# Kernel optimization log

Hardware: AMD Instinct MI355X
Metric: run time of the kernel (lower is better)

## Reference

```python
import jax, jax.numpy as jnp
import numpy as np
import math

B, S, H, NH, NKV, D, I, LCK = 2, 1024, 2048, 32, 8, 64, 8192, 3
EPS = 1e-6
THETA = 10000.0


def rms_norm(x, w, eps=EPS):
    xf = x.astype(jnp.float32)
    var = jnp.mean(xf * xf, axis=-1, keepdims=True)
    return (w * (xf * jax.lax.rsqrt(var + eps))).astype(x.dtype)


def rotate_half(x):
    d = x.shape[-1] // 2
    return jnp.concatenate([-x[..., d:], x[..., :d]], axis=-1)


def setup_inputs() -> dict:
    key = jax.random.key(0)
    ks = jax.random.split(key, 16)
    sc = 0.02
    inp = {
        'input_emb': jax.random.normal(ks[0], (B, S, H), jnp.float32),
        'hidden_states': jax.random.normal(ks[1], (B, S, H), jnp.float32),
        'cache_k': jax.random.normal(ks[2], (LCK, B, NH, S, D), jnp.float32),
        'cache_v': jax.random.normal(ks[3], (LCK, B, NH, S, D), jnp.float32),
    }
    neg = jnp.finfo(jnp.float32).min
    causal = jnp.where(jnp.tril(jnp.ones((S, S), bool)), 0.0, neg).astype(jnp.float32)
    inp['attention_mask'] = jnp.broadcast_to(causal[None, None], (B, 1, S, S))
    inp['position_ids'] = jnp.broadcast_to(jnp.arange(S, dtype=jnp.int32)[None], (B, S))
    inp['wq'] = jax.random.normal(ks[4], (NH * D, 2 * H), jnp.float32) * sc
    inp['wk'] = jax.random.normal(ks[5], (NKV * D, 2 * H), jnp.float32) * sc
    inp['wv'] = jax.random.normal(ks[6], (NKV * D, 2 * H), jnp.float32) * sc
    inp['wo'] = jax.random.normal(ks[7], (H, NH * D), jnp.float32) * sc
    inp['w_gate'] = jax.random.normal(ks[8], (I, H), jnp.float32) * sc
    inp['w_up'] = jax.random.normal(ks[9], (I, H), jnp.float32) * sc
    inp['w_down'] = jax.random.normal(ks[10], (H, I), jnp.float32) * sc
    inp['hidden_norm_w'] = jnp.ones((H,), jnp.float32)
    inp['input_ln_w'] = jnp.ones((H,), jnp.float32)
    inp['post_ln_w'] = jnp.ones((H,), jnp.float32)
    return inp


def _forward(input_emb, hidden_states, cache_k, cache_v, attention_mask, position_ids,
             wq, wk, wv, wo, w_gate, w_up, w_down, hidden_norm_w, input_ln_w, post_ln_w):
    residual = hidden_states
    h = rms_norm(hidden_states, hidden_norm_w)
    e = rms_norm(input_emb, input_ln_w)
    x = jnp.concatenate([e, h], axis=-1)  # [B,S,2H]

    q = jnp.einsum('bsi,oi->bso', x, wq).reshape(B, S, NH, D).transpose(0, 2, 1, 3)
    k = jnp.einsum('bsi,oi->bso', x, wk).reshape(B, S, NKV, D).transpose(0, 2, 1, 3)
    v = jnp.einsum('bsi,oi->bso', x, wv).reshape(B, S, NKV, D).transpose(0, 2, 1, 3)

    # RoPE table up to seq_len = S + LCK, indexed at position_ids + LCK
    inv_freq = 1.0 / (THETA ** (jnp.arange(0, D, 2, dtype=jnp.float32) / D))
    t = jnp.arange(S + LCK, dtype=jnp.float32)
    freqs = t[:, None] * inv_freq[None, :]
    emb = jnp.concatenate([freqs, freqs], axis=-1)  # [S+LCK, D]
    pos = position_ids + LCK
    cos = jnp.cos(emb)[pos][:, None]  # [B,1,S,D]
    sin = jnp.sin(emb)[pos][:, None]
    q = q * cos + rotate_half(q) * sin
    k = k * cos + rotate_half(k) * sin

    n_rep = NH // NKV
    k = jnp.repeat(k, n_rep, axis=1)  # [B,NH,S,D]
    v = jnp.repeat(v, n_rep, axis=1)

    scale = 1.0 / math.sqrt(D)
    # full causal attention against the oldest cache entry
    s0 = jnp.einsum('bhqd,bhkd->bhqk', q, cache_k[0]) * scale + attention_mask
    # diagonal (same-position) attention against remaining cache entries + current keys
    extra_k = jnp.concatenate([cache_k[1:], k[None]], axis=0)  # [LCK,B,NH,S,D]
    extra_v = jnp.concatenate([cache_v[1:], v[None]], axis=0)
    sd = jnp.einsum('bhqd,nbhqd->bhqn', q, extra_k) * scale  # [B,NH,S,LCK]

    attn = jax.nn.softmax(jnp.concatenate([s0, sd], axis=-1).astype(jnp.float32), axis=-1).astype(q.dtype)
    out = jnp.einsum('bhqk,bhkd->bhqd', attn[..., :S], cache_v[0])
    out = out + jnp.einsum('bhqn,nbhqd->bhqd', attn[..., S:], extra_v)
    out = out.transpose(0, 2, 1, 3).reshape(B, S, NH * D)
    attn_out = jnp.einsum('bsi,oi->bso', out, wo)

    h2 = residual + attn_out
    hn = rms_norm(h2, post_ln_w)
    mlp = jnp.einsum('bsi,oi->bso', jax.nn.silu(jnp.einsum('bsi,oi->bso', hn, w_gate)) * jnp.einsum('bsi,oi->bso', hn, w_up), w_down)
    return h2 + mlp


def reference(input_emb, hidden_states, cache_k, cache_v, attention_mask, position_ids,
              wq, wk, wv, wo, w_gate, w_up, w_down, hidden_norm_w, input_ln_w, post_ln_w):
    return _forward(input_emb, hidden_states, cache_k, cache_v, attention_mask, position_ids,
                    wq, wk, wv, wo, w_gate, w_up, w_down, hidden_norm_w, input_ln_w, post_ln_w)
```

## Files before the change

kernel.cpp:

```cpp
#include <hip/hip_runtime.h>
#include <math.h>

#define B_   2
#define S_   1024
#define H_   2048
#define NH_  32
#define NKV_ 8
#define D_   64
#define I_   8192
#define LCK_ 3
#define M_   (B_ * S_)

typedef unsigned short u16;
typedef unsigned int   u32;
typedef __attribute__((ext_vector_type(8))) short bf16x8;
typedef __attribute__((ext_vector_type(4))) float f32x4;
typedef __attribute__((ext_vector_type(2))) unsigned int u32x2;

__device__ __forceinline__ u16 f2b(float f) {
  u32 u = __float_as_uint(f);
  u += 0x7fffu + ((u >> 16) & 1u);
  return (u16)(u >> 16);
}
__device__ __forceinline__ float b2f(u16 h) { return __uint_as_float(((u32)h) << 16); }

__device__ __forceinline__ void st_bf4(u16* p, float a, float b, float c, float d) {
  u32x2 v;
  v.x = (u32)f2b(a) | ((u32)f2b(b) << 16);
  v.y = (u32)f2b(c) | ((u32)f2b(d) << 16);
  *(u32x2*)p = v;
}

__device__ __forceinline__ void cvt16(const float4& a, const float4& b,
                                      const float4& c, const float4& d,
                                      bf16x8& lo, bf16x8& hi) {
  lo[0] = (short)f2b(a.x); lo[1] = (short)f2b(a.y); lo[2] = (short)f2b(a.z); lo[3] = (short)f2b(a.w);
  lo[4] = (short)f2b(b.x); lo[5] = (short)f2b(b.y); lo[6] = (short)f2b(b.z); lo[7] = (short)f2b(b.w);
  hi[0] = (short)f2b(c.x); hi[1] = (short)f2b(c.y); hi[2] = (short)f2b(c.z); hi[3] = (short)f2b(c.w);
  hi[4] = (short)f2b(d.x); hi[5] = (short)f2b(d.y); hi[6] = (short)f2b(d.z); hi[7] = (short)f2b(d.w);
}

__device__ __forceinline__ void async16(const void* g, void* l) {
  __builtin_amdgcn_global_load_lds(
      (const __attribute__((address_space(1))) unsigned int*)(uintptr_t)g,
      (__attribute__((address_space(3))) unsigned int*)(unsigned int)(uintptr_t)l,
      16, 0, 0);
}

__global__ __launch_bounds__(256) void norm_concat_kernel(
    const float* __restrict__ emb, const float* __restrict__ hid,
    const float* __restrict__ w_e, const float* __restrict__ w_h,
    u16* __restrict__ x)
{
  const int row = blockIdx.x;
  const int t = threadIdx.x;
  const float* e = emb + (size_t)row * H_;
  const float* h = hid + (size_t)row * H_;

  const float4 ev0 = *(const float4*)&e[t * 4];
  const float4 ev1 = *(const float4*)&e[t * 4 + 1024];
  const float4 hv0 = *(const float4*)&h[t * 4];
  const float4 hv1 = *(const float4*)&h[t * 4 + 1024];

  float se = ev0.x*ev0.x + ev0.y*ev0.y + ev0.z*ev0.z + ev0.w*ev0.w
           + ev1.x*ev1.x + ev1.y*ev1.y + ev1.z*ev1.z + ev1.w*ev1.w;
  float sh = hv0.x*hv0.x + hv0.y*hv0.y + hv0.z*hv0.z + hv0.w*hv0.w
           + hv1.x*hv1.x + hv1.y*hv1.y + hv1.z*hv1.z + hv1.w*hv1.w;

  #pragma unroll
  for (int m = 1; m < 64; m <<= 1) {
    se += __shfl_xor(se, m);
    sh += __shfl_xor(sh, m);
  }
  __shared__ float red[8];
  const int wv = t >> 6;
  if ((t & 63) == 0) { red[wv] = se; red[4 + wv] = sh; }
  __syncthreads();
  se = red[0] + red[1] + red[2] + red[3];
  sh = red[4] + red[5] + red[6] + red[7];

  const float re = 1.0f / sqrtf(se * (1.0f / H_) + 1e-6f);
  const float rh = 1.0f / sqrtf(sh * (1.0f / H_) + 1e-6f);

  const float4 we0 = *(const float4*)&w_e[t * 4];
  const float4 we1 = *(const float4*)&w_e[t * 4 + 1024];
  const float4 wh0 = *(const float4*)&w_h[t * 4];
  const float4 wh1 = *(const float4*)&w_h[t * 4 + 1024];

  u16* xr = x + (size_t)row * (2 * H_);
  st_bf4(&xr[t * 4],        ev0.x*re*we0.x, ev0.y*re*we0.y, ev0.z*re*we0.z, ev0.w*re*we0.w);
  st_bf4(&xr[t * 4 + 1024], ev1.x*re*we1.x, ev1.y*re*we1.y, ev1.z*re*we1.z, ev1.w*re*we1.w);
  st_bf4(&xr[2048 + t * 4],        hv0.x*rh*wh0.x, hv0.y*rh*wh0.y, hv0.z*rh*wh0.z, hv0.w*rh*wh0.w);
  st_bf4(&xr[2048 + t * 4 + 1024], hv1.x*rh*wh1.x, hv1.y*rh*wh1.y, hv1.z*rh*wh1.z, hv1.w*rh*wh1.w);
}

__global__ __launch_bounds__(256) void rmsnorm_kernel(
    const float* __restrict__ in, const float* __restrict__ w, u16* __restrict__ outp)
{
  const int row = blockIdx.x;
  const int t = threadIdx.x;
  const float* p = in + (size_t)row * H_;
  const float4 v0 = *(const float4*)&p[t * 4];
  const float4 v1 = *(const float4*)&p[t * 4 + 1024];
  float s = v0.x*v0.x + v0.y*v0.y + v0.z*v0.z + v0.w*v0.w
          + v1.x*v1.x + v1.y*v1.y + v1.z*v1.z + v1.w*v1.w;
  #pragma unroll
  for (int m = 1; m < 64; m <<= 1) s += __shfl_xor(s, m);
  __shared__ float red[4];
  const int wv = t >> 6;
  if ((t & 63) == 0) red[wv] = s;
  __syncthreads();
  s = red[0] + red[1] + red[2] + red[3];
  const float rs = 1.0f / sqrtf(s * (1.0f / H_) + 1e-6f);

  const float4 w0 = *(const float4*)&w[t * 4];
  const float4 w1 = *(const float4*)&w[t * 4 + 1024];
  u16* orow = outp + (size_t)row * H_;
  st_bf4(&orow[t * 4],        v0.x*rs*w0.x, v0.y*rs*w0.y, v0.z*rs*w0.z, v0.w*rs*w0.w);
  st_bf4(&orow[t * 4 + 1024], v1.x*rs*w1.x, v1.y*rs*w1.y, v1.z*rs*w1.z, v1.w*rs*w1.w);
}

__global__ __launch_bounds__(256) void convert6_kernel(
    const float* __restrict__ wq, const float* __restrict__ wk, const float* __restrict__ wv,
    const float* __restrict__ wo, const float* __restrict__ wg, const float* __restrict__ wu,
    u16* __restrict__ dst)
{
  const size_t i8 = ((size_t)blockIdx.x * 256 + threadIdx.x) * 8;
  const float* s; size_t base;
  if      (i8 <  8388608) { s = wq; base = 0; }
  else if (i8 < 10485760) { s = wk; base = 8388608; }
  else if (i8 < 12582912) { s = wv; base = 10485760; }
  else if (i8 < 16777216) { s = wo; base = 12582912; }
  else if (i8 < 33554432) { s = wg; base = 16777216; }
  else                    { s = wu; base = 33554432; }
  const float4 a = *(const float4*)&s[i8 - base];
  const float4 b = *(const float4*)&s[i8 - base + 4];
  bf16x8 r;
  r[0] = (short)f2b(a.x); r[1] = (short)f2b(a.y); r[2] = (short)f2b(a.z); r[3] = (short)f2b(a.w);
  r[4] = (short)f2b(b.x); r[5] = (short)f2b(b.y); r[6] = (short)f2b(b.z); r[7] = (short)f2b(b.w);
  *(bf16x8*)&dst[i8] = r;
}

__global__ __launch_bounds__(256) void convert1_kernel(
    const float* __restrict__ src, u16* __restrict__ dst)
{
  const size_t i8 = ((size_t)blockIdx.x * 256 + threadIdx.x) * 8;
  const float4 a = *(const float4*)&src[i8];
  const float4 b = *(const float4*)&src[i8 + 4];
  bf16x8 r;
  r[0] = (short)f2b(a.x); r[1] = (short)f2b(a.y); r[2] = (short)f2b(a.z); r[3] = (short)f2b(a.w);
  r[4] = (short)f2b(b.x); r[5] = (short)f2b(b.y); r[6] = (short)f2b(b.z); r[7] = (short)f2b(b.w);
  *(bf16x8*)&dst[i8] = r;
}

template <int MODE>
__global__ __launch_bounds__(256) void gemm_bf16_kernel(
    const u16* __restrict__ A, const u16* __restrict__ Bw,
    void* Cv, const void* Xv, int M, int N, int K)
{
  __shared__ __align__(16) u16 As[4][128 * 32];
  __shared__ __align__(16) u16 Bs[4][128 * 32];
  const int t = threadIdx.x;
  const int lane = t & 63;
  const int w = t >> 6;
  const int wr = w >> 1, wc = w & 1;
  const int row0 = blockIdx.y * 128;
  const int col0 = blockIdx.x * 128;
  const int kz = blockIdx.z;
  const int Kc = K / (int)gridDim.z;
  const int nsteps = Kc >> 5;

  f32x4 acc[4][4];
  #pragma unroll
  for (int i = 0; i < 4; ++i)
    #pragma unroll
    for (int j = 0; j < 4; ++j)
      #pragma unroll
      for (int r = 0; r < 4; ++r) acc[i][j][r] = 0.f;

  const int srow = lane >> 2;
  const int skc  = (lane & 3) * 8;
  const u16* Ag = A  + (size_t)(row0 + w * 32 + srow) * K + skc + (size_t)kz * Kc;
  const u16* Bg = Bw + (size_t)(col0 + w * 32 + srow) * K + skc + (size_t)kz * Kc;
  const int wofs = w * 1024;

  const int fr = lane & 15;
  const int fq = (lane >> 4) * 8;

  auto stageTo = [&](int k0, u16* ab, u16* bb) {
    async16(Ag + k0,                  ab + wofs);
    async16(Ag + k0 + (size_t)16 * K, ab + wofs + 512);
    async16(Bg + k0,                  bb + wofs);
    async16(Bg + k0 + (size_t)16 * K, bb + wofs + 512);
  };
  auto compute = [&](const u16* asb, const u16* bsb) {
    bf16x8 af[4], bfr[4];
    #pragma unroll
    for (int ti = 0; ti < 4; ++ti)
      af[ti] = *(const bf16x8*)&asb[(wr * 64 + ti * 16 + fr) * 32 + fq];
    #pragma unroll
    for (int tj = 0; tj < 4; ++tj)
      bfr[tj] = *(const bf16x8*)&bsb[(wc * 64 + tj * 16 + fr) * 32 + fq];
    #pragma unroll
    for (int ti = 0; ti < 4; ++ti)
      #pragma unroll
      for (int tj = 0; tj < 4; ++tj)
        acc[ti][tj] = __builtin_amdgcn_mfma_f32_16x16x32_bf16(af[ti], bfr[tj], acc[ti][tj], 0, 0, 0);
  };

  u16 *A0 = &As[0][0], *A1 = &As[1][0], *A2 = &As[2][0], *A3 = &As[3][0];
  u16 *B0 = &Bs[0][0], *B1 = &Bs[1][0], *B2 = &Bs[2][0], *B3 = &Bs[3][0];

  stageTo(0,  A0, B0);
  stageTo(32, A1, B1);
  stageTo(64, A2, B2);

  for (int kt = 0; kt < nsteps; ++kt) {
    const int rem = nsteps - 1 - kt;
    if (rem >= 2)      asm volatile("s_waitcnt vmcnt(8) lgkmcnt(0)" ::: "memory");
    else if (rem == 1) asm volatile("s_waitcnt vmcnt(4) lgkmcnt(0)" ::: "memory");
    else               asm volatile("s_waitcnt vmcnt(0) lgkmcnt(0)" ::: "memory");
    __builtin_amdgcn_s_barrier();
    if (kt + 3 < nsteps) stageTo((kt + 3) * 32, A3, B3);
    compute(A0, B0);
    u16* ta = A0; A0 = A1; A1 = A2; A2 = A3; A3 = ta;
    u16* tb = B0; B0 = B1; B1 = B2; B2 = B3; B3 = tb;
  }

  float* Cf = (float*)Cv + (size_t)kz * ((size_t)M * N);
  u16*  Cb = (u16*)Cv;
  const float* Xf = (const float*)Xv;
  const u16*  Xb = (const u16*)Xv;
  const int rbase = (lane >> 4) * 4;
  const int cofs  = lane & 15;
  #pragma unroll
  for (int ti = 0; ti < 4; ++ti) {
    #pragma unroll
    for (int r = 0; r < 4; ++r) {
      const int gr = row0 + wr * 64 + ti * 16 + rbase + r;
      #pragma unroll
      for (int tj = 0; tj < 4; ++tj) {
        const int gc = col0 + wc * 64 + tj * 16 + cofs;
        const size_t off = (size_t)gr * N + gc;
        const float v = acc[ti][tj][r];
        if constexpr (MODE == 0) {
          Cf[off] = v;
        } else if constexpr (MODE == 1) {
          Cf[off] = v + Xf[off];
        } else if constexpr (MODE == 2) {
          Cb[off] = f2b(v);
        } else {
          const float g = b2f(Xb[off]);
          Cb[off] = f2b((g / (1.f + __expf(-g))) * v);
        }
      }
    }
  }
}

template <int NP>
__global__ __launch_bounds__(256) void reduce_kernel(
    const float* __restrict__ p, const float* __restrict__ resid,
    float* __restrict__ out, size_t nper)
{
  const size_t i = ((size_t)blockIdx.x * 256 + threadIdx.x) * 4;
  float4 s = *(const float4*)&p[i];
  #pragma unroll
  for (int z = 1; z < NP; ++z) {
    const float4 a = *(const float4*)&p[(size_t)z * nper + i];
    s.x += a.x; s.y += a.y; s.z += a.z; s.w += a.w;
  }
  if (resid) {
    const float4 r = *(const float4*)&resid[i];
    s.x += r.x; s.y += r.y; s.z += r.z; s.w += r.w;
  }
  *(float4*)&out[i] = s;
}

__global__ __launch_bounds__(256) void rope_kernel(
    float* __restrict__ qkv, const int* __restrict__ pid)
{
  const int idx = blockIdx.x * 256 + threadIdx.x;
  const int total = M_ * (NH_ + NKV_) * 32;
  if (idx >= total) return;
  const int row = idx / 1280;
  const int rem = idx - row * 1280;
  const int head = rem >> 5;
  const int i = rem & 31;
  const int col = (head < NH_) ? head * 64 : 2048 + (head - NH_) * 64;
  float* base = qkv + (size_t)row * 3072 + col;
  const int pos = pid[row] + LCK_;
  const float invf = exp2f((float)i * (-13.2877123795494f / 32.0f));
  const float ang = (float)pos * invf;
  float sn, c;
  __sincosf(ang, &sn, &c);
  const float x0 = base[i];
  const float x1 = base[i + 32];
  base[i]      = x0 * c - x1 * sn;
  base[i + 32] = x1 * c + x0 * sn;
}

__global__ __launch_bounds__(256) void attn_kernel(
    const float* __restrict__ qkv,
    const float* __restrict__ ck, const float* __restrict__ cv,
    u16* __restrict__ ao)
{
  const int bid = blockIdx.x;
  const int qt = bid & 15;
  const int bh = bid >> 4;
  const int h = bh & 31;
  const int b = bh >> 5;
  const int t = threadIdx.x;
  const int lane = t & 63;
  const int w = t >> 6;
  const int qbase = qt * 64;

  const int fr = lane & 15;
  const int fq = (lane >> 4) * 8;
  const int rbase = (lane >> 4) * 4;
  const int cofs = lane & 15;

  __shared__ __align__(16) u16 Qs[64 * 72];
  __shared__ __align__(16) u16 Ks[64 * 72];
  __shared__ __align__(16) u16 Vts[64 * 72];
  __shared__ __align__(16) u16 Ps[64 * 72];
  __shared__ float Ls[192];

  const size_t bh_off = (size_t)b * NH_ + h;
  const float* K0 = ck + bh_off * S_ * D_;
  const float* V0 = cv + bh_off * S_ * D_;

  const int sr = t >> 2;
  const int sc = (t & 3) * 16;
  {
    const float* qg = qkv + (size_t)(b * S_ + qbase + sr) * 3072 + h * 64 + sc;
    float4 a = *(const float4*)&qg[0], bb = *(const float4*)&qg[4],
           c = *(const float4*)&qg[8], d = *(const float4*)&qg[12];
    a.x*=0.125f; a.y*=0.125f; a.z*=0.125f; a.w*=0.125f;
    bb.x*=0.125f; bb.y*=0.125f; bb.z*=0.125f; bb.w*=0.125f;
    c.x*=0.125f; c.y*=0.125f; c.z*=0.125f; c.w*=0.125f;
    d.x*=0.125f; d.y*=0.125f; d.z*=0.125f; d.w*=0.125f;
    bf16x8 lo, hi; cvt16(a, bb, c, d, lo, hi);
    *(bf16x8*)&Qs[sr * 72 + sc] = lo;
    *(bf16x8*)&Qs[sr * 72 + sc + 8] = hi;
  }

  float m_r[4], l_r[4];
  f32x4 Oacc[4];
  #pragma unroll
  for (int r = 0; r < 4; ++r) { m_r[r] = -3.0e38f; l_r[r] = 0.f; }
  #pragma unroll
  for (int dt = 0; dt < 4; ++dt)
    #pragma unroll
    for (int r = 0; r < 4; ++r) Oacc[dt][r] = 0.f;

  for (int kt = 0; kt <= qt; ++kt) {
    __syncthreads();
    {
      const float* kg = K0 + (size_t)(kt * 64 + sr) * D_ + sc;
      float4 a = *(const float4*)&kg[0], bb = *(const float4*)&kg[4],
             c = *(const float4*)&kg[8], d = *(const float4*)&kg[12];
      bf16x8 lo, hi; cvt16(a, bb, c, d, lo, hi);
      *(bf16x8*)&Ks[sr * 72 + sc] = lo;
      *(bf16x8*)&Ks[sr * 72 + sc + 8] = hi;
      const float* vg = V0 + (size_t)(kt * 64 + sr) * D_ + sc;
      float4 va = *(const float4*)&vg[0], vb4 = *(const float4*)&vg[4],
             vc = *(const float4*)&vg[8], vd = *(const float4*)&vg[12];
      const float vv[16] = {va.x,va.y,va.z,va.w, vb4.x,vb4.y,vb4.z,vb4.w,
                            vc.x,vc.y,vc.z,vc.w, vd.x,vd.y,vd.z,vd.w};
      #pragma unroll
      for (int i = 0; i < 16; ++i) Vts[(sc + i) * 72 + sr] = f2b(vv[i]);
    }
    __syncthreads();

    const bf16x8 qa0 = *(const bf16x8*)&Qs[(w * 16 + fr) * 72 + fq];
    const bf16x8 qa1 = *(const bf16x8*)&Qs[(w * 16 + fr) * 72 + 32 + fq];
    f32x4 sacc[4];
    #pragma unroll
    for (int nt = 0; nt < 4; ++nt) {
      const bf16x8 kb0 = *(const bf16x8*)&Ks[(nt * 16 + fr) * 72 + fq];
      const bf16x8 kb1 = *(const bf16x8*)&Ks[(nt * 16 + fr) * 72 + 32 + fq];
      f32x4 z; z[0]=0.f; z[1]=0.f; z[2]=0.f; z[3]=0.f;
      z = __builtin_amdgcn_mfma_f32_16x16x32_bf16(qa0, kb0, z, 0, 0, 0);
      sacc[nt] = __builtin_amdgcn_mfma_f32_16x16x32_bf16(qa1, kb1, z, 0, 0, 0);
    }
    if (kt == qt) {
      #pragma unroll
      for (int nt = 0; nt < 4; ++nt) {
        const int key = nt * 16 + cofs;
        #pragma unroll
        for (int r = 0; r < 4; ++r)
          if (key > w * 16 + rbase + r) sacc[nt][r] = -3.0e38f;
      }
    }

    #pragma unroll
    for (int r = 0; r < 4; ++r) {
      float rm = fmaxf(fmaxf(sacc[0][r], sacc[1][r]), fmaxf(sacc[2][r], sacc[3][r]));
      rm = fmaxf(rm, __shfl_xor(rm, 1));
      rm = fmaxf(rm, __shfl_xor(rm, 2));
      rm = fmaxf(rm, __shfl_xor(rm, 4));
      rm = fmaxf(rm, __shfl_xor(rm, 8));
      const float mnew = fmaxf(m_r[r], rm);
      const float alpha = __expf(m_r[r] - mnew);
      float p0 = __expf(sacc[0][r] - mnew);
      float p1 = __expf(sacc[1][r] - mnew);
      float p2 = __expf(sacc[2][r] - mnew);
      float p3 = __expf(sacc[3][r] - mnew);
      float rs = p0 + p1 + p2 + p3;
      rs += __shfl_xor(rs, 1);
      rs += __shfl_xor(rs, 2);
      rs += __shfl_xor(rs, 4);
      rs += __shfl_xor(rs, 8);
      l_r[r] = l_r[r] * alpha + rs;
      m_r[r] = mnew;
      #pragma unroll
      for (int dt = 0; dt < 4; ++dt) Oacc[dt][r] *= alpha;
      u16* prow = &Ps[(w * 16 + rbase + r) * 72 + cofs];
      prow[0]  = f2b(p0);
      prow[16] = f2b(p1);
      prow[32] = f2b(p2);
      prow[48] = f2b(p3);
    }

    const bf16x8 pa0 = *(const bf16x8*)&Ps[(w * 16 + fr) * 72 + fq];
    const bf16x8 pa1 = *(const bf16x8*)&Ps[(w * 16 + fr) * 72 + 32 + fq];
    #pragma unroll
    for (int dt = 0; dt < 4; ++dt) {
      const bf16x8 vb0 = *(const bf16x8*)&Vts[(dt * 16 + fr) * 72 + fq];
      const bf16x8 vb1 = *(const bf16x8*)&Vts[(dt * 16 + fr) * 72 + 32 + fq];
      Oacc[dt] = __builtin_amdgcn_mfma_f32_16x16x32_bf16(pa0, vb0, Oacc[dt], 0, 0, 0);
      Oacc[dt] = __builtin_amdgcn_mfma_f32_16x16x32_bf16(pa1, vb1, Oacc[dt], 0, 0, 0);
    }
  }

  if (t < 192) {
    const int n = t >> 6;
    const int r = t & 63;
    const int qp = qbase + r;
    const float* kp;
    if (n < 2) kp = ck + ((((size_t)(n + 1) * B_ + b) * NH_ + h) * S_ + qp) * D_;
    else       kp = qkv + (size_t)(b * S_ + qp) * 3072 + 2048 + (h >> 2) * 64;
    float e = 0.f;
    #pragma unroll 16
    for (int d = 0; d < 64; ++d) e = fmaf(b2f(Qs[r * 72 + d]), kp[d], e);
    Ls[n * 64 + r] = e;
  }
  __syncthreads();

  #pragma unroll
  for (int r = 0; r < 4; ++r) {
    const int qr = w * 16 + rbase + r;
    const int qp = qbase + qr;
    const float e0 = Ls[qr], e1 = Ls[64 + qr], e2 = Ls[128 + qr];
    const float mnew = fmaxf(fmaxf(m_r[r], e0), fmaxf(e1, e2));
    const float alpha = __expf(m_r[r] - mnew);
    const float p0 = __expf(e0 - mnew);
    const float p1 = __expf(e1 - mnew);
    const float p2 = __expf(e2 - mnew);
    const float inv = 1.0f / (l_r[r] * alpha + p0 + p1 + p2);
    const float* v1p = cv + ((((size_t)1 * B_ + b) * NH_ + h) * S_ + qp) * D_;
    const float* v2p = cv + ((((size_t)2 * B_ + b) * NH_ + h) * S_ + qp) * D_;
    const float* v3p = qkv + (size_t)(b * S_ + qp) * 3072 + 2560 + (h >> 2) * 64;
    u16* aorow = ao + (size_t)(b * S_ + qp) * 2048 + h * 64;
    #pragma unroll
    for (int dt = 0; dt < 4; ++dt) {
      const int col = dt * 16 + cofs;
      const float o = (Oacc[dt][r] * alpha + p0 * v1p[col] + p1 * v2p[col] + p2 * v3p[col]) * inv;
      aorow[col] = f2b(o);
    }
  }
}

extern "C" void kernel_launch(void* const* d_in, const int* in_sizes, int n_in,
                              void* d_out, int out_size, void* d_ws, size_t ws_size,
                              hipStream_t stream)
{
  const float* input_emb = (const float*)d_in[0];
  const float* hidden    = (const float*)d_in[1];
  const float* cache_k   = (const float*)d_in[2];
  const float* cache_v   = (const float*)d_in[3];
  const int*   pos_ids   = (const int*)d_in[5];
  const float* wq = (const float*)d_in[6];
  const float* wk = (const float*)d_in[7];
  const float* wv = (const float*)d_in[8];
  const float* wo = (const float*)d_in[9];
  const float* wg = (const float*)d_in[10];
  const float* wu = (const float*)d_in[11];
  const float* wd = (const float*)d_in[12];
  const float* w_hidden_norm = (const float*)d_in[13];
  const float* w_input_ln    = (const float*)d_in[14];
  const float* w_post_ln     = (const float*)d_in[15];
  float* out = (float*)d_out;

  char* wsb = (char*)d_ws;
  u16*   wall   = (u16*)(wsb + 0);
  u16*   wqkv_b = wall;
  u16*   wo_b   = (u16*)(wsb + 25165824);
  u16*   wg_b   = (u16*)(wsb + 33554432);
  u16*   wu_b   = (u16*)(wsb + 67108864);
  u16*   xb     = (u16*)(wsb + 100663296);
  float* qkvf   = (float*)(wsb + 117440512);
  u16*   ao     = (u16*)(wsb + 142606336);
  float* h2     = (float*)(wsb + 150994944);
  u16*   hn     = (u16*)(wsb + 100663296);
  u16*   gbb    = (u16*)(wsb + 117440512);
  u16*   gub    = (u16*)(wsb + 0);
  u16*   wd_b   = (u16*)(wsb + 33554432);
  float* wo_p   = (float*)(wsb + 100663296);
  float* dn_p   = (float*)(wsb + 67108864);

  convert6_kernel<<<24576, 256, 0, stream>>>(wq, wk, wv, wo, wg, wu, wall);
  norm_concat_kernel<<<M_, 256, 0, stream>>>(input_emb, hidden, w_input_ln, w_hidden_norm, xb);
  gemm_bf16_kernel<0><<<dim3(24, 16, 2), 256, 0, stream>>>(xb, wqkv_b, qkvf, nullptr, M_, 3072, 4096);
  reduce_kernel<2><<<6144, 256, 0, stream>>>(qkvf, nullptr, qkvf, (size_t)M_ * 3072);
  rope_kernel<<<10240, 256, 0, stream>>>(qkvf, pos_ids);
  attn_kernel<<<B_ * NH_ * (S_ / 64), 256, 0, stream>>>(qkvf, cache_k, cache_v, ao);
  gemm_bf16_kernel<0><<<dim3(16, 16, 2), 256, 0, stream>>>(ao, wo_b, wo_p, nullptr, M_, 2048, 2048);
  reduce_kernel<2><<<4096, 256, 0, stream>>>(wo_p, hidden, h2, (size_t)M_ * 2048);
  rmsnorm_kernel<<<M_, 256, 0, stream>>>(h2, w_post_ln, hn);
  gemm_bf16_kernel<2><<<dim3(64, 16), 256, 0, stream>>>(hn, wg_b, gbb, nullptr, M_, 8192, 2048);
  convert1_kernel<<<8192, 256, 0, stream>>>(wd, wd_b);
  gemm_bf16_kernel<3><<<dim3(64, 16), 256, 0, stream>>>(hn, wu_b, gub, gbb, M_, 8192, 2048);
  gemm_bf16_kernel<0><<<dim3(16, 16, 4), 256, 0, stream>>>(gub, wd_b, dn_p, nullptr, M_, 2048, 8192);
  reduce_kernel<4><<<4096, 256, 0, stream>>>(dn_p, h2, out, (size_t)M_ * 2048);
}
```

Baseline: 878.6 us.

## Add 256x256-tile 4-stage pipelined bf16 MFMA GEMM for QKV and MLP projections

Introduces a 512-thread GEMM kernel that computes a 256x256 output tile per block. It uses a 4-buffer async global-to-LDS pipeline, interleaves the loads for the next stages between MFMA groups, and raises wave priority with s_setprio around the MFMA groups. The QKV, gate, up and down projections now use this kernel with grids resized to match. The larger tile is meant to improve operand reuse and hide memory latency. In exchange it needs about 128KB of LDS per block, which limits occupancy to one block per CU, and the QKV launch yields only 192 blocks, which can leave some CUs idle.

```diff
diff --git a/kernel.cpp b/kernel.cpp
--- a/kernel.cpp
+++ b/kernel.cpp
@@ -243,6 +243,149 @@
         const int gc = col0 + wc * 64 + tj * 16 + cofs;
         const size_t off = (size_t)gr * N + gc;
         const float v = acc[ti][tj][r];
+        if constexpr (MODE == 0) {
+          Cf[off] = v;
+        } else if constexpr (MODE == 1) {
+          Cf[off] = v + Xf[off];
+        } else if constexpr (MODE == 2) {
+          Cb[off] = f2b(v);
+        } else {
+          const float g = b2f(Xb[off]);
+          Cb[off] = f2b((g / (1.f + __expf(-g))) * v);
+        }
+      }
+    }
+  }
+}
+
+#define MM8(AF0, AF1, M0)                                                            \
+  acc[M0][0]   = __builtin_amdgcn_mfma_f32_16x16x32_bf16(AF0, b0, acc[M0][0], 0,0,0);   \
+  acc[M0][1]   = __builtin_amdgcn_mfma_f32_16x16x32_bf16(AF0, b1, acc[M0][1], 0,0,0);   \
+  acc[M0][2]   = __builtin_amdgcn_mfma_f32_16x16x32_bf16(AF0, b2, acc[M0][2], 0,0,0);   \
+  acc[M0][3]   = __builtin_amdgcn_mfma_f32_16x16x32_bf16(AF0, b3, acc[M0][3], 0,0,0);   \
+  acc[M0+1][0] = __builtin_amdgcn_mfma_f32_16x16x32_bf16(AF1, b0, acc[M0+1][0], 0,0,0); \
+  acc[M0+1][1] = __builtin_amdgcn_mfma_f32_16x16x32_bf16(AF1, b1, acc[M0+1][1], 0,0,0); \
+  acc[M0+1][2] = __builtin_amdgcn_mfma_f32_16x16x32_bf16(AF1, b2, acc[M0+1][2], 0,0,0); \
+  acc[M0+1][3] = __builtin_amdgcn_mfma_f32_16x16x32_bf16(AF1, b3, acc[M0+1][3], 0,0,0);
+
+template <int MODE>
+__global__ __launch_bounds__(512, 2) void gemm256_bf16_kernel(
+    const u16* __restrict__ A, const u16* __restrict__ Bw,
+    void* Cv, const void* Xv, int M, int N, int K)
+{
+  __shared__ __align__(16) u16 As[4][256 * 32];
+  __shared__ __align__(16) u16 Bs[4][256 * 32];
+  const int t = threadIdx.x;
+  const int lane = t & 63;
+  const int w = t >> 6;
+  const int wr = w >> 2, wc = w & 3;
+  const int row0 = blockIdx.y * 256;
+  const int col0 = blockIdx.x * 256;
+  const int kz = blockIdx.z;
+  const int Kc = K / (int)gridDim.z;
+  const int nsteps = Kc >> 5;
+
+  f32x4 acc[8][4];
+  #pragma unroll
+  for (int i = 0; i < 8; ++i)
+    #pragma unroll
+    for (int j = 0; j < 4; ++j)
+      #pragma unroll
+      for (int r = 0; r < 4; ++r) acc[i][j][r] = 0.f;
+
+  const int srow = lane >> 2;
+  const int skc  = (lane & 3) * 8;
+  const u16* Ag = A  + (size_t)(row0 + w * 32 + srow) * K + skc + (size_t)kz * Kc;
+  const u16* Bg = Bw + (size_t)(col0 + w * 32 + srow) * K + skc + (size_t)kz * Kc;
+  const int wofs = w * 1024;
+
+  const int fr = lane & 15;
+  const int fq = (lane >> 4) * 8;
+
+  u16 *A0 = &As[0][0], *A1 = &As[1][0], *A2 = &As[2][0], *A3 = &As[3][0];
+  u16 *B0 = &Bs[0][0], *B1 = &Bs[1][0], *B2 = &Bs[2][0], *B3 = &Bs[3][0];
+
+  auto stageAll = [&](int k0, u16* ab, u16* bb) {
+    async16(Ag + k0,                  ab + wofs);
+    async16(Ag + k0 + (size_t)16 * K, ab + wofs + 512);
+    async16(Bg + k0,                  bb + wofs);
+    async16(Bg + k0 + (size_t)16 * K, bb + wofs + 512);
+  };
+
+  stageAll(0,  A0, B0);
+  stageAll(32, A1, B1);
+  stageAll(64, A2, B2);
+
+  for (int kt = 0; kt < nsteps; ++kt) {
+    const int rem = nsteps - 1 - kt;
+    if (rem >= 2)      asm volatile("s_waitcnt vmcnt(8) lgkmcnt(0)" ::: "memory");
+    else if (rem == 1) asm volatile("s_waitcnt vmcnt(4) lgkmcnt(0)" ::: "memory");
+    else               asm volatile("s_waitcnt vmcnt(0) lgkmcnt(0)" ::: "memory");
+    __builtin_amdgcn_s_barrier();
+    const bool doStage = (kt + 3 < nsteps);
+    const int ks = (kt + 3) * 32;
+
+    const bf16x8 b0 = *(const bf16x8*)&B0[(wc * 64 +  0 + fr) * 32 + fq];
+    const bf16x8 b1 = *(const bf16x8*)&B0[(wc * 64 + 16 + fr) * 32 + fq];
+    const bf16x8 b2 = *(const bf16x8*)&B0[(wc * 64 + 32 + fr) * 32 + fq];
+    const bf16x8 b3 = *(const bf16x8*)&B0[(wc * 64 + 48 + fr) * 32 + fq];
+
+    {
+      const bf16x8 a0 = *(const bf16x8*)&A0[(wr * 128 +  0 + fr) * 32 + fq];
+      const bf16x8 a1 = *(const bf16x8*)&A0[(wr * 128 + 16 + fr) * 32 + fq];
+      if (doStage) async16(Ag + ks, A3 + wofs);
+      __builtin_amdgcn_s_setprio(1);
+      MM8(a0, a1, 0)
+      __builtin_amdgcn_s_setprio(0);
+    }
+    __builtin_amdgcn_s_barrier();
+    {
+      const bf16x8 a0 = *(const bf16x8*)&A0[(wr * 128 + 32 + fr) * 32 + fq];
+      const bf16x8 a1 = *(const bf16x8*)&A0[(wr * 128 + 48 + fr) * 32 + fq];
+      if (doStage) async16(Ag + ks + (size_t)16 * K, A3 + wofs + 512);
+      __builtin_amdgcn_s_setprio(1);
+      MM8(a0, a1, 2)
+      __builtin_amdgcn_s_setprio(0);
+    }
+    __builtin_amdgcn_s_barrier();
+    {
+      const bf16x8 a0 = *(const bf16x8*)&A0[(wr * 128 + 64 + fr) * 32 + fq];
+      const bf16x8 a1 = *(const bf16x8*)&A0[(wr * 128 + 80 + fr) * 32 + fq];
+      if (doStage) async16(Bg + ks, B3 + wofs);
+      __builtin_amdgcn_s_setprio(1);
+      MM8(a0, a1, 4)
+      __builtin_amdgcn_s_setprio(0);
+    }
+    __builtin_amdgcn_s_barrier();
+    {
+      const bf16x8 a0 = *(const bf16x8*)&A0[(wr * 128 +  96 + fr) * 32 + fq];
+      const bf16x8 a1 = *(const bf16x8*)&A0[(wr * 128 + 112 + fr) * 32 + fq];
+      if (doStage) async16(Bg + ks + (size_t)16 * K, B3 + wofs + 512);
+      __builtin_amdgcn_s_setprio(1);
+      MM8(a0, a1, 6)
+      __builtin_amdgcn_s_setprio(0);
+    }
+
+    u16* ta = A0; A0 = A1; A1 = A2; A2 = A3; A3 = ta;
+    u16* tb = B0; B0 = B1; B1 = B2; B2 = B3; B3 = tb;
+  }
+
+  float* Cf = (float*)Cv + (size_t)kz * ((size_t)M * N);
+  u16*  Cb = (u16*)Cv;
+  const float* Xf = (const float*)Xv;
+  const u16*  Xb = (const u16*)Xv;
+  const int rbase = (lane >> 4) * 4;
+  const int cofs  = lane & 15;
+  #pragma unroll
+  for (int m = 0; m < 8; ++m) {
+    #pragma unroll
+    for (int r = 0; r < 4; ++r) {
+      const int gr = row0 + wr * 128 + m * 16 + rbase + r;
+      #pragma unroll
+      for (int n = 0; n < 4; ++n) {
+        const int gc = col0 + wc * 64 + n * 16 + cofs;
+        const size_t off = (size_t)gr * N + gc;
+        const float v = acc[m][n][r];
         if constexpr (MODE == 0) {
           Cf[off] = v;
         } else if constexpr (MODE == 1) {
@@ -512,16 +655,16 @@
 
   convert6_kernel<<<24576, 256, 0, stream>>>(wq, wk, wv, wo, wg, wu, wall);
   norm_concat_kernel<<<M_, 256, 0, stream>>>(input_emb, hidden, w_input_ln, w_hidden_norm, xb);
-  gemm_bf16_kernel<0><<<dim3(24, 16, 2), 256, 0, stream>>>(xb, wqkv_b, qkvf, nullptr, M_, 3072, 4096);
+  gemm256_bf16_kernel<0><<<dim3(12, 8, 2), 512, 0, stream>>>(xb, wqkv_b, qkvf, nullptr, M_, 3072, 4096);
   reduce_kernel<2><<<6144, 256, 0, stream>>>(qkvf, nullptr, qkvf, (size_t)M_ * 3072);
   rope_kernel<<<10240, 256, 0, stream>>>(qkvf, pos_ids);
   attn_kernel<<<B_ * NH_ * (S_ / 64), 256, 0, stream>>>(qkvf, cache_k, cache_v, ao);
   gemm_bf16_kernel<0><<<dim3(16, 16, 2), 256, 0, stream>>>(ao, wo_b, wo_p, nullptr, M_, 2048, 2048);
   reduce_kernel<2><<<4096, 256, 0, stream>>>(wo_p, hidden, h2, (size_t)M_ * 2048);
   rmsnorm_kernel<<<M_, 256, 0, stream>>>(h2, w_post_ln, hn);
-  gemm_bf16_kernel<2><<<dim3(64, 16), 256, 0, stream>>>(hn, wg_b, gbb, nullptr, M_, 8192, 2048);
+  gemm256_bf16_kernel<2><<<dim3(32, 8), 512, 0, stream>>>(hn, wg_b, gbb, nullptr, M_, 8192, 2048);
   convert1_kernel<<<8192, 256, 0, stream>>>(wd, wd_b);
-  gemm_bf16_kernel<3><<<dim3(64, 16), 256, 0, stream>>>(hn, wu_b, gub, gbb, M_, 8192, 2048);
-  gemm_bf16_kernel<0><<<dim3(16, 16, 4), 256, 0, stream>>>(gub, wd_b, dn_p, nullptr, M_, 2048, 8192);
+  gemm256_bf16_kernel<3><<<dim3(32, 8), 512, 0, stream>>>(hn, wu_b, gub, gbb, M_, 8192, 2048);
+  gemm256_bf16_kernel<0><<<dim3(8, 8, 4), 512, 0, stream>>>(gub, wd_b, dn_p, nullptr, M_, 2048, 8192);
   reduce_kernel<4><<<4096, 256, 0, stream>>>(dn_p, h2, out, (size_t)M_ * 2048);
 }
```

Result: faster. 825.0 us (-6.1%).
